# Optimization experiments

Measured on AMD Instinct MI355X. Metric: run time of the kernel, lower is better.

## Reference

```python
import jax, jax.numpy as jnp
import numpy as np

B, T, C, E = 2, 100, 80, 32
MH = MW = 64
IN_H = IN_W = 640.0
IOU_FACTOR, CLS_FACTOR, TOPK = 6.0, 0.5, 10
EPS = 1e-9


def get_anchors_and_scalers(fmaps, in_h, in_w):
    anchors, scalers = [], []
    for fh, fw in fmaps:
        stride = in_h / fh
        ys = (np.arange(fh) + 0.5) * stride
        xs = (np.arange(fw) + 0.5) * stride
        gy, gx = np.meshgrid(ys, xs, indexing='ij')
        anchors.append(np.stack([gx, gy], -1).reshape(-1, 2))
        scalers.append(np.full(fh * fw, stride))
    return (np.concatenate(anchors).astype(np.float32),
            np.concatenate(scalers).astype(np.float32))


def setup_inputs() -> dict:
    key = jax.random.key(0)
    ks = jax.random.split(key, 8)
    anchors_np, scalers_np = get_anchors_and_scalers([(80, 80), (40, 40), (20, 20)], IN_H, IN_W)
    anchors = jnp.asarray(anchors_np)
    scalers = jnp.asarray(scalers_np)
    A = anchors.shape[0]
    cls_logits = jax.random.normal(ks[0], (B, A, C), jnp.float32)
    wh = jax.random.uniform(ks[1], (B, A, 2), jnp.float32, 16.0, 160.0)
    ctr = anchors[None] + jax.random.normal(ks[2], (B, A, 2), jnp.float32) * 8.0
    pred_boxes = jnp.clip(jnp.concatenate([ctr - wh / 2, ctr + wh / 2], -1), 0.0, IN_W)
    mask_embs = jax.random.normal(ks[3], (B, A, E), jnp.float32)
    protos = jax.random.normal(ks[4], (B, MH, MW, E), jnp.float32)
    tl = jax.random.uniform(ks[5], (B, T, 2), jnp.float32, 0.0, 560.0)
    twh = jax.random.uniform(ks[6], (B, T, 2), jnp.float32, 30.0, 240.0)
    target_bbox = jnp.concatenate([tl, jnp.minimum(tl + twh, IN_W)], -1)
    target_cls = jax.random.randint(ks[7], (B, T), 0, C, jnp.int32)
    target_masks = (jax.random.uniform(jax.random.fold_in(key, 7), (B, MH, MW, T)) > 0.5).astype(jnp.float32)
    return {'cls_logits': cls_logits, 'pred_boxes': pred_boxes, 'mask_embs': mask_embs,
            'protos': protos, 'target_cls': target_cls, 'target_bbox': target_bbox,
            'target_masks': target_masks, 'anchors': anchors, 'scalers': scalers}


def _ciou_pairwise(gt, pr):
    # gt [B,T,4], pr [B,A,4] -> [B,T,A]
    g = gt[:, :, None, :]
    p = pr[:, None, :, :]
    ix1 = jnp.maximum(g[..., 0], p[..., 0]); iy1 = jnp.maximum(g[..., 1], p[..., 1])
    ix2 = jnp.minimum(g[..., 2], p[..., 2]); iy2 = jnp.minimum(g[..., 3], p[..., 3])
    inter = jnp.clip(ix2 - ix1, 0.0) * jnp.clip(iy2 - iy1, 0.0)
    wg = g[..., 2] - g[..., 0]; hg = g[..., 3] - g[..., 1]
    wp = p[..., 2] - p[..., 0]; hp = p[..., 3] - p[..., 1]
    union = wg * hg + wp * hp - inter + EPS
    iou = inter / union
    cw = jnp.maximum(g[..., 2], p[..., 2]) - jnp.minimum(g[..., 0], p[..., 0])
    ch = jnp.maximum(g[..., 3], p[..., 3]) - jnp.minimum(g[..., 1], p[..., 1])
    c2 = cw * cw + ch * ch + EPS
    rho2 = ((g[..., 0] + g[..., 2] - p[..., 0] - p[..., 2]) ** 2 +
            (g[..., 1] + g[..., 3] - p[..., 1] - p[..., 3]) ** 2) / 4.0
    v = (4.0 / (jnp.pi ** 2)) * (jnp.arctan(wg / (hg + EPS)) - jnp.arctan(wp / (hp + EPS))) ** 2
    alpha = jax.lax.stop_gradient(v / (1.0 - iou + v + EPS))
    return iou - rho2 / c2 - alpha * v


def _bbox_mask(boxes, mh, mw, in_h, in_w):
    # boxes [B,A,4] pixel xyxy -> [B,A,mh,mw] binary inside-box mask on mask grid
    sx, sy = mw / in_w, mh / in_h
    x1, y1, x2, y2 = boxes[..., 0] * sx, boxes[..., 1] * sy, boxes[..., 2] * sx, boxes[..., 3] * sy
    rows = jnp.arange(mh, dtype=boxes.dtype)
    cols = jnp.arange(mw, dtype=boxes.dtype)
    rm = (rows >= y1[..., None]) & (rows < y2[..., None])  # [B,A,mh]
    cm = (cols >= x1[..., None]) & (cols < x2[..., None])  # [B,A,mw]
    return (rm[..., :, None] & cm[..., None, :]).astype(boxes.dtype)


def _assign_and_build(cls_logits, pred_boxes, mask_embs, protos,
                      target_cls, target_bbox, target_masks, anchors, scalers):
    Bn, A, Cn = cls_logits.shape
    mh, mw = protos.shape[1], protos.shape[2]
    # --- task-aligned assigner ---
    lt, rb = target_bbox[:, :, None, :2], target_bbox[:, :, None, 2:]
    deltas = jnp.concatenate([anchors[None, None] - lt, rb - anchors[None, None]], -1)
    grid_mask = (jnp.min(deltas, -1) > 0).astype(cls_logits.dtype)  # [B,T,A]
    iou_mat = jnp.clip(_ciou_pairwise(target_bbox, pred_boxes), 0.0, 1.0)  # [B,T,A]
    cls_prob = jax.nn.sigmoid(cls_logits)  # [B,A,C]
    oh_t = jax.nn.one_hot(target_cls, Cn, dtype=cls_prob.dtype)  # [B,T,C]
    cls_mat = jnp.einsum('btc,bac->bta', oh_t, cls_prob)  # [B,T,A]
    tmat = grid_mask * (iou_mat ** IOU_FACTOR) * (cls_mat ** CLS_FACTOR)
    kth = jax.lax.top_k(tmat, TOPK)[0][..., -1:]  # [B,T,1]
    topk_targets = jnp.where((tmat >= kth) & (tmat > 0), tmat, 0.0)
    unique_idx = jnp.argmax(topk_targets, axis=1)  # [B,A] best GT per anchor
    valid = (jnp.sum(topk_targets, axis=1) > 0).astype(cls_logits.dtype)  # [B,A]
    align_bbox = jnp.take_along_axis(target_bbox, jnp.broadcast_to(unique_idx[..., None], (Bn, A, 4)), axis=1)
    align_cls_idx = jnp.take_along_axis(target_cls, unique_idx, axis=1)  # [B,A]
    max_target = jnp.max(tmat, axis=-1, keepdims=True)
    max_iou = jnp.max(iou_mat, axis=-1, keepdims=True)
    norm_term = tmat / (max_target + EPS) * max_iou  # [B,T,A]
    norm_g = jnp.take_along_axis(jnp.transpose(norm_term, (0, 2, 1)), unique_idx[..., None], axis=2)  # [B,A,1]
    align_cls = jax.nn.one_hot(align_cls_idx, Cn, dtype=cls_logits.dtype) * norm_g * valid[..., None]
    # --- loss-target assembly (compute_loss body) ---
    align_bbox_scaled = align_bbox / scalers[None, :, None]
    boxes_scaled = pred_boxes / scalers[None, :, None]
    box_target = jnp.concatenate([align_bbox_scaled, valid[..., None], align_cls], -1)
    box_mask = _bbox_mask(align_bbox, mh, mw, IN_H, IN_W)  # [B,A,mh,mw]
    valid_seg = box_mask * valid[..., None, None]
    seg_pred = jax.nn.sigmoid(jnp.einsum('bne,bhwe->bnhw', mask_embs, protos)) * valid_seg
    seg_pred = seg_pred.reshape(Bn, A, mh * mw)
    masks_t = jnp.transpose(target_masks, (0, 3, 1, 2))  # [B,T,mh,mw]
    idx4 = jnp.broadcast_to(unique_idx[..., None, None], (Bn, A, mh, mw))
    align_seg = (jnp.take_along_axis(masks_t, idx4, axis=1) * valid_seg).reshape(Bn, A, mh * mw)
    area = ((align_bbox[..., 2] - align_bbox[..., 0]) * (align_bbox[..., 3] - align_bbox[..., 1])
            / (IN_W * IN_H))
    seg_target = jnp.concatenate([area[..., None], valid[..., None], align_seg], -1)
    return jnp.concatenate([boxes_scaled, cls_logits, box_target, seg_pred, seg_target], -1)


def reference(cls_logits, pred_boxes, mask_embs, protos, target_cls, target_bbox,
              target_masks, anchors, scalers):
    return _assign_and_build(cls_logits, pred_boxes, mask_embs, protos,
                             target_cls, target_bbox, target_masks, anchors, scalers)
```

## Files before the change

### kernel.cpp

```cpp
#include <hip/hip_runtime.h>
#include <math.h>

#define A_TOT 8400
#define B_N   2
#define T_N   100
#define C_N   80
#define E_N   32
#define MH_N  64
#define MW_N  64
#define ROW_N 8363
#define NROWS (B_N*A_TOT)
#define EPSF  1e-9f
#define PARAM_STRIDE 12
#define COMP_CAP 1536
#define NEGINF -1e30f

typedef float vfloat4 __attribute__((ext_vector_type(4)));

__global__ __launch_bounds__(256) void k_prep(
    const float* __restrict__ pred_boxes, const float* __restrict__ target_bbox,
    float* __restrict__ pred_atan, float* __restrict__ tgt_atan) {
  int i = blockIdx.x * 256 + threadIdx.x;
  if (i < NROWS) {
    float4 pb = *(const float4*)(pred_boxes + (size_t)i*4);
    pred_atan[i] = atanf((pb.z - pb.x) / ((pb.w - pb.y) + EPSF));
  }
  if (i < B_N*T_N) {
    float4 g = *(const float4*)(target_bbox + i*4);
    tgt_atan[i] = atanf((g.z - g.x) / ((g.w - g.y) + EPSF));
  }
}

__device__ __forceinline__ float2 tmat_eval(
    float gx1, float gy1, float gx2, float gy2,
    float ax,  float ay,
    float px1, float py1, float px2, float py2,
    float cl, float atg, float atp) {
  float ix1 = fmaxf(gx1,px1), iy1 = fmaxf(gy1,py1);
  float ix2 = fminf(gx2,px2), iy2 = fminf(gy2,py2);
  float inter = fmaxf(ix2-ix1,0.f) * fmaxf(iy2-iy1,0.f);
  float wg = gx2-gx1, hg = gy2-gy1, wp = px2-px1, hp = py2-py1;
  float uni = wg*hg + wp*hp - inter + EPSF;
  float iou = inter / uni;
  float cw = fmaxf(gx2,px2) - fminf(gx1,px1);
  float ch = fmaxf(gy2,py2) - fminf(gy1,py1);
  float c2 = cw*cw + ch*ch + EPSF;
  float dx = gx1+gx2-px1-px2, dy = gy1+gy2-py1-py2;
  float rho2 = (dx*dx + dy*dy) * 0.25f;
  float da = atg - atp;
  float v  = 0.4052847345693511f * da * da;
  float alpha = v / (1.f - iou + v + EPSF);
  float ciou = iou - rho2/c2 - alpha*v;
  float iouc = fminf(fmaxf(ciou, 0.f), 1.f);

  float tm = 0.f;
  if (ax > gx1 && ay > gy1 && ax < gx2 && ay < gy2) {
    float cp = 1.f / (1.f + expf(-cl));
    float i2 = iouc * iouc;
    tm = i2*i2*i2 * sqrtf(cp);
  }
  return make_float2(tm, iouc);
}

__global__ __launch_bounds__(512) void k_score(
    const float* __restrict__ cls_logits, const float* __restrict__ pred_boxes,
    const float* __restrict__ target_bbox, const int* __restrict__ target_cls,
    const float* __restrict__ anchors,
    const float* __restrict__ pred_atan, const float* __restrict__ tgt_atan,
    float* __restrict__ tmat,
    float* __restrict__ kth, float* __restrict__ maxt, float* __restrict__ maxiou) {
  int bt   = blockIdx.x;
  int b    = bt / T_N;
  int tid  = threadIdx.x;
  int lane = tid & 63, wid = tid >> 6;
  __shared__ float comp[COMP_CAP];
  __shared__ float redm[8], redi[8];
  __shared__ float wtop[8][10];
  __shared__ int   cnt;
  if (tid == 0) cnt = 0;
  __syncthreads();

  float4 g  = *(const float4*)(target_bbox + bt*4);
  int    tc = target_cls[bt];
  float atg = tgt_atan[bt];
  float* trow = tmat + (size_t)bt * A_TOT;

  float lm = 0.f, li = 0.f;
  for (int a = tid; a < A_TOT; a += 512) {
    float ax = anchors[a*2+0], ay = anchors[a*2+1];
    float4 pb = *(const float4*)(pred_boxes + ((size_t)(b*A_TOT+a))*4);
    float cl = cls_logits[((size_t)(b*A_TOT+a))*C_N + tc];
    float2 r = tmat_eval(g.x,g.y,g.z,g.w, ax,ay, pb.x,pb.y,pb.z,pb.w,
                         cl, atg, pred_atan[b*A_TOT + a]);
    trow[a] = r.x;
    li = fmaxf(li, r.y);
    if (r.x > 0.f) {
      lm = fmaxf(lm, r.x);
      comp[atomicAdd(&cnt, 1)] = r.x;
    }
  }
  #pragma unroll
  for (int off = 32; off; off >>= 1) {
    lm = fmaxf(lm, __shfl_xor(lm, off));
    li = fmaxf(li, __shfl_xor(li, off));
  }
  if (lane == 0) { redm[wid] = lm; redi[wid] = li; }
  __syncthreads();
  if (tid == 0) {
    float m = redm[0], mi = redi[0];
    #pragma unroll
    for (int w = 1; w < 8; w++) { m = fmaxf(m, redm[w]); mi = fmaxf(mi, redi[w]); }
    maxt[bt] = m; maxiou[bt] = mi;
  }
  int count = cnt;

  int base = wid*64 + lane;
  float e0 = (base        < count) ? comp[base]        : NEGINF;
  float e1 = (base + 512  < count) ? comp[base + 512]  : NEGINF;
  float e2 = (base + 1024 < count) ? comp[base + 1024] : NEGINF;
  float mytop = NEGINF;
  #pragma unroll
  for (int k = 0; k < 10; k++) {
    float bv = e0; int bs = 0;
    if (e1 > bv) { bv = e1; bs = 1; }
    if (e2 > bv) { bv = e2; bs = 2; }
    float v = bv; int id = (lane << 2) | bs;
    #pragma unroll
    for (int off = 32; off; off >>= 1) {
      float ov = __shfl_xor(v, off); int oid = __shfl_xor(id, off);
      if (ov > v || (ov == v && oid < id)) { v = ov; id = oid; }
    }
    if ((id >> 2) == lane) {
      int s = id & 3;
      if (s == 0) e0 = NEGINF; else if (s == 1) e1 = NEGINF; else e2 = NEGINF;
    }
    if (lane == k) mytop = v;
  }
  if (lane < 10) wtop[wid][lane] = mytop;
  __syncthreads();

  if (wid == 0) {
    int ia = lane, ib = 64 + lane;
    float f0 = wtop[ia/10][ia%10];
    float f1 = (ib < 80) ? wtop[ib/10][ib%10] : NEGINF;
    float cur = NEGINF;
    #pragma unroll
    for (int k = 0; k < 10; k++) {
      float bv = f0; int bs = 0;
      if (f1 > bv) { bv = f1; bs = 1; }
      float v = bv; int id = (lane << 1) | bs;
      #pragma unroll
      for (int off = 32; off; off >>= 1) {
        float ov = __shfl_xor(v, off); int oid = __shfl_xor(id, off);
        if (ov > v || (ov == v && oid < id)) { v = ov; id = oid; }
      }
      if ((id >> 1) == lane) { if ((id & 1) == 0) f0 = NEGINF; else f1 = NEGINF; }
      cur = v;
    }
    if (lane == 0) kth[bt] = fmaxf(cur, 0.f);
  }
}

__global__ __launch_bounds__(64) void k_assign(
    const float* __restrict__ tmat,
    const float* __restrict__ kth, const float* __restrict__ maxt, const float* __restrict__ maxiou,
    const float* __restrict__ target_bbox, const int* __restrict__ target_cls,
    const float* __restrict__ scalers,
    float* __restrict__ params) {
  int b   = blockIdx.y;
  int tid = threadIdx.x;
  int a   = blockIdx.x * 64 + tid;
  __shared__ float kths[T_N];
  for (int i = tid; i < T_N; i += 64) kths[i] = kth[b*T_N + i];
  __syncthreads();
  if (a >= A_TOT) return;

  const float* col = tmat + (size_t)b * T_N * A_TOT + a;
  float best = 0.f; int u = 0, any = 0;
  #pragma unroll 4
  for (int t = 0; t < T_N; t++) {
    float v = col[(size_t)t * A_TOT];
    if (v > 0.f && v >= kths[t]) {
      any = 1;
      if (v > best) { best = v; u = t; }
    }
  }
  int bu = b*T_N + u;
  float ng = any ? best / (maxt[bu] + EPSF) * maxiou[bu] : 0.f;
  float4 tb = *(const float4*)(target_bbox + bu*4);
  float s = scalers[a];
  float area = (tb.z - tb.x) * (tb.w - tb.y) / (640.f*640.f);

  int row = b*A_TOT + a;
  float* pp = params + (size_t)row * PARAM_STRIDE;
  *(float4*)pp       = tb;
  *(float4*)(pp + 4) = make_float4(any ? 1.f : 0.f, ng, s, area);
  *(float4*)(pp + 8) = make_float4(__int_as_float(u), __int_as_float(target_cls[bu]), 0.f, 0.f);
}

__device__ __forceinline__ float val_at(
    unsigned pos, unsigned row, int b,
    const float* __restrict__ cls_logits, const float* __restrict__ pred_boxes,
    const float* __restrict__ mask_embs,  const float* __restrict__ protos,
    const float* __restrict__ t_masks,    const float* __restrict__ params,
    float4 P0, float4 P1) {
  if (pos < 84u) {
    if (pos < 4u) return pred_boxes[(size_t)row*4 + pos] / P1.z;
    return cls_logits[(size_t)row*C_N + (pos-4u)];
  }
  if (pos < 169u) {
    if (pos < 88u) {
      float t = (pos==84u)?P0.x:((pos==85u)?P0.y:((pos==86u)?P0.z:P0.w));
      return t / P1.z;
    }
    if (pos == 88u) return P1.x;
    int c = (int)pos - 89;
    int ct = __float_as_int(params[(size_t)row*PARAM_STRIDE + 9]);
    return (P1.x > 0.5f && c == ct) ? P1.y : 0.f;
  }
  if (pos < 4265u) {
    if (P1.x <= 0.5f) return 0.f;
    unsigned p = pos - 169u; int h = p >> 6, w = p & 63;
    float fh = (float)h, fw = (float)w;
    float x1s = P0.x*0.1f, y1s = P0.y*0.1f, x2s = P0.z*0.1f, y2s = P0.w*0.1f;
    if (!(fh >= y1s && fh < y2s && fw >= x1s && fw < x2s)) return 0.f;
    const float* pr = protos   + ((size_t)((b*MH_N + h)*MW_N + w)) * E_N;
    const float* se = mask_embs + (size_t)row * E_N;
    float acc = 0.f;
    #pragma unroll
    for (int e = 0; e < E_N; e++) acc += se[e] * pr[e];
    return 1.f / (1.f + expf(-acc));
  }
  if (pos == 4265u) return P1.w;
  if (pos == 4266u) return P1.x;
  if (P1.x <= 0.5f) return 0.f;
  unsigned p = pos - 4267u; int h = p >> 6, w = p & 63;
  float fh = (float)h, fw = (float)w;
  float x1s = P0.x*0.1f, y1s = P0.y*0.1f, x2s = P0.z*0.1f, y2s = P0.w*0.1f;
  if (!(fh >= y1s && fh < y2s && fw >= x1s && fw < x2s)) return 0.f;
  int u = __float_as_int(params[(size_t)row*PARAM_STRIDE + 8]);
  return t_masks[((size_t)((b*MH_N + h)*MW_N + w)) * T_N + u];
}

__global__ __launch_bounds__(256) void k_write(
    const float* __restrict__ cls_logits, const float* __restrict__ pred_boxes,
    const float* __restrict__ mask_embs,  const float* __restrict__ protos,
    const float* __restrict__ t_masks,    const float* __restrict__ params,
    float* __restrict__ out) {
  const unsigned total_chunks = (unsigned)NROWS * ROW_N / 4u;
  unsigned idx    = blockIdx.x * 256u + threadIdx.x;
  unsigned stride = gridDim.x * 256u;
  for (unsigned c = idx; c < total_chunks; c += stride) {
    unsigned e0  = c * 4u;
    unsigned row = e0 / (unsigned)ROW_N;
    unsigned pos0 = e0 - row * (unsigned)ROW_N;
    vfloat4 o;
    if (pos0 + 3u < (unsigned)ROW_N) {
      int b = row >= (unsigned)A_TOT;
      const float* pp = params + (size_t)row * PARAM_STRIDE;
      float4 P0 = *(const float4*)pp;
      float4 P1 = *(const float4*)(pp + 4);
      bool pure_seg = (pos0 >= 169u && pos0 + 3u < 4265u) || (pos0 >= 4267u);
      if (P1.x <= 0.5f && pure_seg) {
        o = (vfloat4)(0.f);
      } else {
        o.x = val_at(pos0,    row, b, cls_logits, pred_boxes, mask_embs, protos, t_masks, params, P0, P1);
        o.y = val_at(pos0+1u, row, b, cls_logits, pred_boxes, mask_embs, protos, t_masks, params, P0, P1);
        o.z = val_at(pos0+2u, row, b, cls_logits, pred_boxes, mask_embs, protos, t_masks, params, P0, P1);
        o.w = val_at(pos0+3u, row, b, cls_logits, pred_boxes, mask_embs, protos, t_masks, params, P0, P1);
      }
    } else {
      float tmp[4];
      #pragma unroll
      for (int j = 0; j < 4; j++) {
        unsigned pos = pos0 + j, r = row;
        if (pos >= (unsigned)ROW_N) { pos -= (unsigned)ROW_N; r = row + 1u; }
        int b = r >= (unsigned)A_TOT;
        const float* pp = params + (size_t)r * PARAM_STRIDE;
        float4 P0 = *(const float4*)pp;
        float4 P1 = *(const float4*)(pp + 4);
        tmp[j] = val_at(pos, r, b, cls_logits, pred_boxes, mask_embs, protos, t_masks, params, P0, P1);
      }
      o.x = tmp[0]; o.y = tmp[1]; o.z = tmp[2]; o.w = tmp[3];
    }
    __builtin_nontemporal_store(o, (vfloat4*)(out + (size_t)e0));
  }
}

extern "C" void kernel_launch(void* const* d_in, const int* in_sizes, int n_in,
                              void* d_out, int out_size, void* d_ws, size_t ws_size,
                              hipStream_t stream) {
  const float* cls_logits   = (const float*)d_in[0];
  const float* pred_boxes   = (const float*)d_in[1];
  const float* mask_embs    = (const float*)d_in[2];
  const float* protos       = (const float*)d_in[3];
  const int*   target_cls   = (const int*)  d_in[4];
  const float* target_bbox  = (const float*)d_in[5];
  const float* target_masks = (const float*)d_in[6];
  const float* anchors      = (const float*)d_in[7];
  const float* scalers      = (const float*)d_in[8];
  float* out = (float*)d_out;

  float* ws        = (float*)d_ws;
  float* kth       = ws;
  float* maxt      = kth    + B_N*T_N;
  float* maxiou    = maxt   + B_N*T_N;
  float* params    = ws + 600;
  float* tmat      = params + (size_t)NROWS*PARAM_STRIDE;
  float* pred_atan = tmat + (size_t)B_N*T_N*A_TOT;
  float* tgt_atan  = pred_atan + NROWS;

  k_prep<<<(NROWS + 255)/256, 256, 0, stream>>>(pred_boxes, target_bbox,
                                                pred_atan, tgt_atan);
  k_score<<<B_N*T_N, 512, 0, stream>>>(cls_logits, pred_boxes, target_bbox,
                                       target_cls, anchors, pred_atan, tgt_atan,
                                       tmat, kth, maxt, maxiou);
  dim3 gAsn((A_TOT + 63)/64, B_N);
  k_assign<<<gAsn, 64, 0, stream>>>(tmat, kth, maxt, maxiou, target_bbox,
                                    target_cls, scalers, params);
  k_write<<<2048, 256, 0, stream>>>(cls_logits, pred_boxes, mask_embs, protos,
                                    target_masks, params, out);
}
```

Measured before the change: 182.5 us.

## Zero output with memset and scatter only nonzero entries per row

```diff
diff --git a/kernel.cpp b/kernel.cpp
--- a/kernel.cpp
+++ b/kernel.cpp
@@ -14,8 +14,6 @@
 #define PARAM_STRIDE 12
 #define COMP_CAP 1536
 #define NEGINF -1e30f
-
-typedef float vfloat4 __attribute__((ext_vector_type(4)));
 
 __global__ __launch_bounds__(256) void k_prep(
     const float* __restrict__ pred_boxes, const float* __restrict__ target_bbox,
@@ -198,92 +196,52 @@
   *(float4*)(pp + 8) = make_float4(__int_as_float(u), __int_as_float(target_cls[bu]), 0.f, 0.f);
 }
 
-__device__ __forceinline__ float val_at(
-    unsigned pos, unsigned row, int b,
-    const float* __restrict__ cls_logits, const float* __restrict__ pred_boxes,
-    const float* __restrict__ mask_embs,  const float* __restrict__ protos,
-    const float* __restrict__ t_masks,    const float* __restrict__ params,
-    float4 P0, float4 P1) {
-  if (pos < 84u) {
-    if (pos < 4u) return pred_boxes[(size_t)row*4 + pos] / P1.z;
-    return cls_logits[(size_t)row*C_N + (pos-4u)];
-  }
-  if (pos < 169u) {
-    if (pos < 88u) {
-      float t = (pos==84u)?P0.x:((pos==85u)?P0.y:((pos==86u)?P0.z:P0.w));
-      return t / P1.z;
-    }
-    if (pos == 88u) return P1.x;
-    int c = (int)pos - 89;
-    int ct = __float_as_int(params[(size_t)row*PARAM_STRIDE + 9]);
-    return (P1.x > 0.5f && c == ct) ? P1.y : 0.f;
-  }
-  if (pos < 4265u) {
-    if (P1.x <= 0.5f) return 0.f;
-    unsigned p = pos - 169u; int h = p >> 6, w = p & 63;
-    float fh = (float)h, fw = (float)w;
-    float x1s = P0.x*0.1f, y1s = P0.y*0.1f, x2s = P0.z*0.1f, y2s = P0.w*0.1f;
-    if (!(fh >= y1s && fh < y2s && fw >= x1s && fw < x2s)) return 0.f;
-    const float* pr = protos   + ((size_t)((b*MH_N + h)*MW_N + w)) * E_N;
-    const float* se = mask_embs + (size_t)row * E_N;
-    float acc = 0.f;
-    #pragma unroll
-    for (int e = 0; e < E_N; e++) acc += se[e] * pr[e];
-    return 1.f / (1.f + expf(-acc));
-  }
-  if (pos == 4265u) return P1.w;
-  if (pos == 4266u) return P1.x;
-  if (P1.x <= 0.5f) return 0.f;
-  unsigned p = pos - 4267u; int h = p >> 6, w = p & 63;
-  float fh = (float)h, fw = (float)w;
-  float x1s = P0.x*0.1f, y1s = P0.y*0.1f, x2s = P0.z*0.1f, y2s = P0.w*0.1f;
-  if (!(fh >= y1s && fh < y2s && fw >= x1s && fw < x2s)) return 0.f;
-  int u = __float_as_int(params[(size_t)row*PARAM_STRIDE + 8]);
-  return t_masks[((size_t)((b*MH_N + h)*MW_N + w)) * T_N + u];
-}
-
-__global__ __launch_bounds__(256) void k_write(
+__global__ __launch_bounds__(256) void k_sparse(
     const float* __restrict__ cls_logits, const float* __restrict__ pred_boxes,
     const float* __restrict__ mask_embs,  const float* __restrict__ protos,
     const float* __restrict__ t_masks,    const float* __restrict__ params,
     float* __restrict__ out) {
-  const unsigned total_chunks = (unsigned)NROWS * ROW_N / 4u;
-  unsigned idx    = blockIdx.x * 256u + threadIdx.x;
-  unsigned stride = gridDim.x * 256u;
-  for (unsigned c = idx; c < total_chunks; c += stride) {
-    unsigned e0  = c * 4u;
-    unsigned row = e0 / (unsigned)ROW_N;
-    unsigned pos0 = e0 - row * (unsigned)ROW_N;
-    vfloat4 o;
-    if (pos0 + 3u < (unsigned)ROW_N) {
-      int b = row >= (unsigned)A_TOT;
-      const float* pp = params + (size_t)row * PARAM_STRIDE;
-      float4 P0 = *(const float4*)pp;
-      float4 P1 = *(const float4*)(pp + 4);
-      bool pure_seg = (pos0 >= 169u && pos0 + 3u < 4265u) || (pos0 >= 4267u);
-      if (P1.x <= 0.5f && pure_seg) {
-        o = (vfloat4)(0.f);
-      } else {
-        o.x = val_at(pos0,    row, b, cls_logits, pred_boxes, mask_embs, protos, t_masks, params, P0, P1);
-        o.y = val_at(pos0+1u, row, b, cls_logits, pred_boxes, mask_embs, protos, t_masks, params, P0, P1);
-        o.z = val_at(pos0+2u, row, b, cls_logits, pred_boxes, mask_embs, protos, t_masks, params, P0, P1);
-        o.w = val_at(pos0+3u, row, b, cls_logits, pred_boxes, mask_embs, protos, t_masks, params, P0, P1);
-      }
-    } else {
-      float tmp[4];
+  unsigned row = blockIdx.x;
+  int b   = row >= (unsigned)A_TOT;
+  int tid = threadIdx.x;
+  __shared__ float semb[E_N];
+
+  const float* pp = params + (size_t)row * PARAM_STRIDE;
+  float4 P0 = *(const float4*)pp;
+  float4 P1 = *(const float4*)(pp + 4);
+  int u  = __float_as_int(pp[8]);
+  int ct = __float_as_int(pp[9]);
+  bool valid = P1.x > 0.5f;
+  size_t base = (size_t)row * ROW_N;
+
+  if (tid < 92) {
+    if (tid < 4) out[base + tid] = pred_boxes[(size_t)row*4 + tid] / P1.z;
+    else if (tid < 84) out[base + tid] = cls_logits[(size_t)row*C_N + (tid-4)];
+    else if (tid < 88) {
+      float t = (tid==84)?P0.x:((tid==85)?P0.y:((tid==86)?P0.z:P0.w));
+      out[base + tid] = t / P1.z;
+    }
+    else if (tid == 88) out[base + 88] = P1.x;
+    else if (tid == 89) { if (valid) out[base + 89 + ct] = P1.y; }
+    else if (tid == 90) out[base + 4265] = P1.w;
+    else                out[base + 4266] = P1.x;
+  }
+  if (!valid) return;
+  if (tid < E_N) semb[tid] = mask_embs[(size_t)row * E_N + tid];
+  __syncthreads();
+
+  float x1s = P0.x*0.1f, y1s = P0.y*0.1f, x2s = P0.z*0.1f, y2s = P0.w*0.1f;
+  for (int p = tid; p < MH_N*MW_N; p += 256) {
+    int h = p >> 6, w = p & 63;
+    float fh = (float)h, fw = (float)w;
+    if (fh >= y1s && fh < y2s && fw >= x1s && fw < x2s) {
+      const float* pr = protos + ((size_t)((b*MH_N + h)*MW_N + w)) * E_N;
+      float acc = 0.f;
       #pragma unroll
-      for (int j = 0; j < 4; j++) {
-        unsigned pos = pos0 + j, r = row;
-        if (pos >= (unsigned)ROW_N) { pos -= (unsigned)ROW_N; r = row + 1u; }
-        int b = r >= (unsigned)A_TOT;
-        const float* pp = params + (size_t)r * PARAM_STRIDE;
-        float4 P0 = *(const float4*)pp;
-        float4 P1 = *(const float4*)(pp + 4);
-        tmp[j] = val_at(pos, r, b, cls_logits, pred_boxes, mask_embs, protos, t_masks, params, P0, P1);
-      }
-      o.x = tmp[0]; o.y = tmp[1]; o.z = tmp[2]; o.w = tmp[3];
-    }
-    __builtin_nontemporal_store(o, (vfloat4*)(out + (size_t)e0));
+      for (int e = 0; e < E_N; e++) acc += semb[e] * pr[e];
+      out[base + 169  + p] = 1.f / (1.f + expf(-acc));
+      out[base + 4267 + p] = t_masks[((size_t)((b*MH_N + h)*MW_N + w)) * T_N + u];
+    }
   }
 }
 
@@ -310,6 +268,7 @@
   float* pred_atan = tmat + (size_t)B_N*T_N*A_TOT;
   float* tgt_atan  = pred_atan + NROWS;
 
+  hipMemsetAsync(out, 0, (size_t)NROWS * ROW_N * sizeof(float), stream);
   k_prep<<<(NROWS + 255)/256, 256, 0, stream>>>(pred_boxes, target_bbox,
                                                 pred_atan, tgt_atan);
   k_score<<<B_N*T_N, 512, 0, stream>>>(cls_logits, pred_boxes, target_bbox,
@@ -318,6 +277,6 @@
   dim3 gAsn((A_TOT + 63)/64, B_N);
   k_assign<<<gAsn, 64, 0, stream>>>(tmat, kth, maxt, maxiou, target_bbox,
                                     target_cls, scalers, params);
-  k_write<<<2048, 256, 0, stream>>>(cls_logits, pred_boxes, mask_embs, protos,
-                                    target_masks, params, out);
-}
+  k_sparse<<<NROWS, 256, 0, stream>>>(cls_logits, pred_boxes, mask_embs, protos,
+                                      target_masks, params, out);
+}
```

Result: slower. 190.5 us (+4.4%).
